# Optimization experiments

Measured on AMD Instinct MI355X. Metric: run time of the kernel, lower is better.

The kernel has to match this reference:

```python
import jax, jax.numpy as jnp
import numpy as np

N = 50000      # nodes
E = 800000     # edges (avg degree 16)
NF = 128       # input feature dim
H = 128        # hidden dim
GAMMA = 1.0    # gm init arg
COS_EPS = 1e-8 # F.cosine_similarity eps
EW_MIN = 1e-4  # edge-weight clamp


def setup_inputs() -> dict:
    key = jax.random.key(0)
    ks = jax.random.split(key, 9)
    x = jax.random.normal(ks[0], (N, NF), dtype=jnp.float32)
    edge_index = jax.random.randint(ks[1], (2, E), 0, N, dtype=jnp.int64)
    sensitive_attr = jax.random.randint(ks[2], (N,), 0, 2, dtype=jnp.int64)
    s1 = 1.0 / np.sqrt(NF)
    s2 = 1.0 / np.sqrt(H)
    W1 = jax.random.normal(ks[3], (NF, H), dtype=jnp.float32) * s1
    b1 = jnp.zeros((H,), dtype=jnp.float32)
    W2 = jax.random.normal(ks[4], (H, H), dtype=jnp.float32) * s2
    b2 = jnp.zeros((H,), dtype=jnp.float32)
    Wc = jax.random.normal(ks[5], (H, 1), dtype=jnp.float32) * s2
    bc = jnp.zeros((1,), dtype=jnp.float32)
    return {"x": x, "edge_index": edge_index, "sensitive_attr": sensitive_attr,
            "W1": W1, "b1": b1, "W2": W2, "b2": b2, "Wc": Wc, "bc": bc}


def gcn_conv(x, W, b, src, dst, ew, n):
    """PyG GCNConv: lin -> symmetric-normalized edge-weighted aggregation (+self loops) -> bias."""
    xt = x @ W                                              # [N,H]
    deg = jax.ops.segment_sum(ew, dst, num_segments=n) + 1.0  # self-loop weight 1
    dinv = jnp.where(deg > 0, deg ** -0.5, 0.0)             # [N]
    norm = dinv[src] * ew * dinv[dst]                       # [E]
    agg = jax.ops.segment_sum(xt[src] * norm[:, None], dst, num_segments=n)
    # self-loop contribution: norm_ii = dinv[i] * 1 * dinv[i]
    return agg + xt * (dinv * dinv)[:, None] + b


def reference(x, edge_index, sensitive_attr, W1, b1, W2, b2, Wc, bc):
    src, dst = edge_index[0], edge_index[1]
    # cosine-similarity edge weights (gather-heavy)
    xs, xd = x[src], x[dst]                                  # [E,F] each
    dot = jnp.sum(xs * xd, axis=1)
    ns = jnp.maximum(jnp.sqrt(jnp.sum(xs * xs, axis=1)), COS_EPS)
    nd = jnp.maximum(jnp.sqrt(jnp.sum(xd * xd, axis=1)), COS_EPS)
    sim = dot / (ns * nd)
    sen_diff = (sensitive_attr[src] != sensitive_attr[dst]).astype(x.dtype)
    ew = jnp.maximum(sim * jnp.exp(-GAMMA * sen_diff), EW_MIN)
    # two GCN layers (dropout is identity in eval mode)
    h = jax.nn.relu(gcn_conv(x, W1, b1, src, dst, ew, N))
    h = jax.nn.relu(gcn_conv(h, W2, b2, src, dst, ew, N))
    y = h @ Wc + bc                                          # [N,1]
    return (y, h)
```

## Files before the change

kernel.cpp:

```cpp
#include <hip/hip_runtime.h>


typedef unsigned short u16;
typedef unsigned int u32;
typedef __attribute__((ext_vector_type(8))) short short8;
typedef __attribute__((ext_vector_type(4))) float floatx4;

__device__ __forceinline__ float bflo(u32 u){ return __uint_as_float(u << 16); }
__device__ __forceinline__ float bfhi(u32 u){ return __uint_as_float(u & 0xFFFF0000u); }
__device__ __forceinline__ float bf1(u16 u){ return __uint_as_float(((u32)u) << 16); }
__device__ __forceinline__ u16 f2bf(float f){
    u32 u = __float_as_uint(f);
    u += 0x7FFFu + ((u >> 16) & 1u);
    return (u16)(u >> 16);
}
__device__ __forceinline__ u32 pack2(float a, float b){
    return (u32)f2bf(a) | ((u32)f2bf(b) << 16);
}
__device__ __forceinline__ float wsum(float v){
#pragma unroll
    for (int o = 32; o > 0; o >>= 1) v += __shfl_xor(v, o, 64);
    return v;
}
__device__ __forceinline__ float ld1(const void* p, size_t idx, int f32){
    return f32 ? ((const float*)p)[idx] : bf1(((const u16*)p)[idx]);
}
__device__ __forceinline__ int ldidx(const int* p, size_t i, int i64){
    return i64 ? p[2 * i] : p[i];
}

__global__ void classify_k(const u32* __restrict__ xw, const int* __restrict__ eiw,
                           int* __restrict__ flags)
{
    __shared__ int c_out, c_nz;
    int t = threadIdx.x;
    if (t == 0) { c_out = 0; c_nz = 0; }
    __syncthreads();
    u32 w = xw[t];
    int e = (w >> 7) & 0xFF;
    int outl = (e < 110 || e > 140) ? 1 : 0;
    int nz = (eiw[2 * t + 1] != 0) ? 1 : 0;
    atomicAdd(&c_out, outl);
    atomicAdd(&c_nz, nz);
    __syncthreads();
    if (t == 0) { flags[0] = (c_out > 256); flags[1] = (c_nz < 256); }
}

__global__ __launch_bounds__(256) void convhist_k(const void* __restrict__ x,
                                                  u32* __restrict__ xb,
                                                  float* __restrict__ rn, int N,
                                                  const int* __restrict__ ei,
                                                  int* __restrict__ cnt, int E,
                                                  const int* __restrict__ flags,
                                                  int nbN)
{
    if ((int)blockIdx.x < nbN) {
        int i = blockIdx.x * 4 + (threadIdx.x >> 6);
        if (i >= N) return;
        int lane = threadIdx.x & 63;
        u32 u;
        if (flags[0]) {
            const float* q = (const float*)x + (size_t)i * 128 + lane * 2;
            u = pack2(q[0], q[1]);
        } else u = ((const u32*)x)[(size_t)i * 64 + lane];
        xb[(size_t)i * 64 + lane] = u;
        float f0 = bflo(u), f1 = bfhi(u);
        float ss = wsum(f0 * f0 + f1 * f1);
        if (lane == 0) rn[i] = 1.0f / fmaxf(sqrtf(ss), 1e-8f);
    } else {
        int e = (blockIdx.x - nbN) * 256 + threadIdx.x;
        if (e >= E) return;
        int d = ldidx(ei, (size_t)E + e, flags[1]);
        if ((u32)d >= (u32)N) d = 0;
        atomicAdd(&cnt[d], 1);
    }
}

__global__ void prep_k(const void* __restrict__ W1, const void* __restrict__ W2,
                       uint4* __restrict__ wf1, uint4* __restrict__ wf2,
                       const int* __restrict__ flags)
{
    int slot = blockIdx.x * 256 + threadIdx.x;
    if (slot >= 4096) return;
    int f32w = flags[0];
    const void* W = (slot < 2048) ? W1 : W2;
    uint4* wf = (slot < 2048) ? wf1 : wf2;
    int s = slot & 2047;
    int lane = s & 63, kk = (s >> 6) & 3, ct = s >> 8;
    int q = lane >> 4, n = lane & 15;
    int col = ct * 16 + n, k0 = kk * 32 + q * 8;
    union { u16 us[8]; uint4 u4; } tmp;
#pragma unroll
    for (int j = 0; j < 8; ++j)
        tmp.us[j] = f2bf(ld1(W, (size_t)(k0 + j) * 128 + col, f32w));
    wf[s] = tmp.u4;
}

__global__ __launch_bounds__(256) void scanA_k(int* __restrict__ cnt,
                                               int* __restrict__ rowp,
                                               int* __restrict__ bsum, int N)
{
    __shared__ int wtot[4];
    int t = threadIdx.x, lane = t & 63, w = t >> 6;
    int i0 = blockIdx.x * 1024 + t * 4;
    int v[4];
#pragma unroll
    for (int k = 0; k < 4; ++k) {
        int i = i0 + k;
        v[k] = (i < N) ? cnt[i] : 0;
        if (i < N) cnt[i] = 0;
    }
    int t4 = v[0] + v[1] + v[2] + v[3];
    int sc = t4;
#pragma unroll
    for (int o = 1; o < 64; o <<= 1) {
        int nv = __shfl_up(sc, o);
        if (lane >= o) sc += nv;
    }
    if (lane == 63) wtot[w] = sc;
    __syncthreads();
    int wo = 0, tot = 0;
#pragma unroll
    for (int k = 0; k < 4; ++k) { int s = wtot[k]; if (k < w) wo += s; tot += s; }
    int pre = wo + sc - t4;
#pragma unroll
    for (int k = 0; k < 4; ++k) {
        int i = i0 + k;
        if (i < N) rowp[i] = pre;
        pre += v[k];
    }
    if (t == 0) bsum[blockIdx.x] = tot;
}

__global__ void scanB_k(int* __restrict__ bsum, int* __restrict__ rowp,
                        int nb, int N)
{
    int lane = threadIdx.x;
    int carry = 0;
    for (int base = 0; base < nb; base += 64) {
        int i = base + lane;
        int v = (i < nb) ? bsum[i] : 0;
        int sc = v;
#pragma unroll
        for (int o = 1; o < 64; o <<= 1) {
            int nv = __shfl_up(sc, o);
            if (lane >= o) sc += nv;
        }
        if (i < nb) bsum[i] = carry + sc - v;
        carry += __shfl(sc, 63);
    }
    if (lane == 0) rowp[N] = carry;
}

__global__ __launch_bounds__(256) void scanC_k(int* __restrict__ rowp,
                                               const int* __restrict__ bsum, int N)
{
    int off = bsum[blockIdx.x];
    int i0 = blockIdx.x * 1024 + threadIdx.x * 4;
#pragma unroll
    for (int k = 0; k < 4; ++k) {
        int i = i0 + k;
        if (i < N) rowp[i] += off;
    }
}

__global__ __launch_bounds__(256) void ewscat_k(const u32* __restrict__ xb,
                                                const float* __restrict__ rn,
                                                const int* __restrict__ ei,
                                                const int* __restrict__ sa,
                                                const int* __restrict__ rowp,
                                                int* __restrict__ cnt,
                                                u32* __restrict__ rec,
                                                float* __restrict__ degacc,
                                                int E, int N,
                                                const int* __restrict__ flags)
{
    int t = threadIdx.x;
    int lane = t & 63;
    int g = lane >> 4, j = lane & 15;
    int wid = (blockIdx.x * 256 + t) >> 6;
    int eb = wid * 16;
    int i64 = flags[1];
    int sArr[4], dArr[4];
    bool ok[4];
#pragma unroll
    for (int k = 0; k < 4; ++k) {
        int e = eb + k * 4 + g;
        ok[k] = e < E;
        int s = 0, d = 0;
        if (ok[k]) {
            s = ldidx(ei, e, i64); d = ldidx(ei, (size_t)E + e, i64);
            if ((u32)s >= (u32)N) s = 0;
            if ((u32)d >= (u32)N) d = 0;
        }
        sArr[k] = s; dArr[k] = d;
    }
    uint4 A[4], B[4];
#pragma unroll
    for (int k = 0; k < 4; ++k) {
        A[k] = ((const uint4*)(xb + (size_t)sArr[k] * 64))[j];
        B[k] = ((const uint4*)(xb + (size_t)dArr[k] * 64))[j];
    }
    float dot[4];
#pragma unroll
    for (int k = 0; k < 4; ++k) {
        dot[k] = bflo(A[k].x) * bflo(B[k].x) + bfhi(A[k].x) * bfhi(B[k].x)
               + bflo(A[k].y) * bflo(B[k].y) + bfhi(A[k].y) * bfhi(B[k].y)
               + bflo(A[k].z) * bflo(B[k].z) + bfhi(A[k].z) * bfhi(B[k].z)
               + bflo(A[k].w) * bflo(B[k].w) + bfhi(A[k].w) * bfhi(B[k].w);
    }
#pragma unroll
    for (int o = 8; o > 0; o >>= 1) {
#pragma unroll
        for (int k = 0; k < 4; ++k) dot[k] += __shfl_xor(dot[k], o);
    }
    if (j == 0) {
#pragma unroll
        for (int k = 0; k < 4; ++k) {
            if (!ok[k]) continue;
            int s = sArr[k], d = dArr[k];
            float sim = dot[k] * rn[s] * rn[d];
            int as_ = i64 ? sa[2 * (size_t)s] : sa[s];
            int ad_ = i64 ? sa[2 * (size_t)d] : sa[d];
            float f = (as_ != ad_) ? 0.36787944117144233f : 1.0f;
            float w = fmaxf(sim * f, 1e-4f);
            int pos = rowp[d] + atomicAdd(&cnt[d], 1);
            if ((u32)pos >= (u32)E) pos = 0;
            rec[pos] = ((u32)s << 16) | f2bf(w);
            atomicAdd(&degacc[d], w);
        }
    }
}

__global__ __launch_bounds__(256) void dinv_k(float* __restrict__ dv, int N)
{
    int i = blockIdx.x * 256 + threadIdx.x;
    if (i < N) dv[i] = 1.0f / sqrtf(1.0f + dv[i]);
}

__global__ __launch_bounds__(256) void agg_k(const u32* __restrict__ feat,
                                             const int* __restrict__ rowp,
                                             const u32* __restrict__ rec,
                                             const float* __restrict__ dinv,
                                             u32* __restrict__ Tb, int N, int E)
{
    int i = blockIdx.x * 4 + (threadIdx.x >> 6);
    if (i >= N) return;
    int lane = threadIdx.x & 63;
    float di = dinv[i], sc = di * di;
    u32 u = feat[(size_t)i * 64 + lane];
    float a0 = bflo(u) * sc, a1 = bfhi(u) * sc;
    int p0 = rowp[i], p1 = rowp[i + 1];
    if (p0 < 0) p0 = 0;
    if (p1 > E) p1 = E;
    int p = p0;
    for (; p + 7 < p1; p += 8) {
        u32 r[8]; int s[8]; u32 v[8];
#pragma unroll
        for (int k = 0; k < 8; ++k) {
            r[k] = rec[p + k];
            s[k] = r[k] >> 16;
            if (s[k] >= N) s[k] = 0;
        }
#pragma unroll
        for (int k = 0; k < 8; ++k) v[k] = feat[(size_t)s[k] * 64 + lane];
#pragma unroll
        for (int k = 0; k < 8; ++k) {
            float w = bf1((u16)r[k]) * di * dinv[s[k]];
            a0 = fmaf(w, bflo(v[k]), a0);
            a1 = fmaf(w, bfhi(v[k]), a1);
        }
    }
    for (; p + 1 < p1; p += 2) {
        u32 r0 = rec[p], r1 = rec[p + 1];
        int s0 = r0 >> 16, s1 = r1 >> 16;
        if (s0 >= N) s0 = 0;
        if (s1 >= N) s1 = 0;
        u32 v0 = feat[(size_t)s0 * 64 + lane];
        u32 v1 = feat[(size_t)s1 * 64 + lane];
        float w0 = bf1((u16)r0) * di * dinv[s0];
        float w1 = bf1((u16)r1) * di * dinv[s1];
        a0 = fmaf(w0, bflo(v0), a0); a1 = fmaf(w0, bfhi(v0), a1);
        a0 = fmaf(w1, bflo(v1), a0); a1 = fmaf(w1, bfhi(v1), a1);
    }
    if (p < p1) {
        u32 r0 = rec[p];
        int s0 = r0 >> 16;
        if (s0 >= N) s0 = 0;
        u32 v0 = feat[(size_t)s0 * 64 + lane];
        float w0 = bf1((u16)r0) * di * dinv[s0];
        a0 = fmaf(w0, bflo(v0), a0); a1 = fmaf(w0, bfhi(v0), a1);
    }
    Tb[(size_t)i * 64 + lane] = pack2(a0, a1);
}

__global__ __launch_bounds__(256) void gemm_m(const u32* __restrict__ Tb,
                                              const uint4* __restrict__ wfrag,
                                              const void* __restrict__ bias,
                                              void* __restrict__ out, int outbf,
                                              int N,
                                              const void* __restrict__ Wc,
                                              const void* __restrict__ bc,
                                              float* __restrict__ yout,
                                              const int* __restrict__ flags)
{
    int t = threadIdx.x, wave = t >> 6, lane = t & 63;
    int q = lane >> 4, n = lane & 15;
    int f32w = flags[0];
    int rowbase = blockIdx.x * 64 + wave * 16;
    int arow = rowbase + n; if (arow > N - 1) arow = N - 1;
    const uint4* ap = (const uint4*)(Tb + (size_t)arow * 64);
    short8 a[4];
#pragma unroll
    for (int kk = 0; kk < 4; ++kk) {
        uint4 av = ap[kk * 4 + q];
        a[kk] = *(short8*)&av;
    }
    floatx4 acc[8];
#pragma unroll
    for (int ct = 0; ct < 8; ++ct) acc[ct] = (floatx4){0.f, 0.f, 0.f, 0.f};
#pragma unroll
    for (int ct = 0; ct < 8; ++ct) {
#pragma unroll
        for (int kk = 0; kk < 4; ++kk) {
            uint4 bv = wfrag[(ct * 4 + kk) * 64 + lane];
            acc[ct] = __builtin_amdgcn_mfma_f32_16x16x32_bf16(
                a[kk], *(short8*)&bv, acc[ct], 0, 0, 0);
        }
    }
    float bcv = 0.0f;
    float part[4] = {0.f, 0.f, 0.f, 0.f};
    if (yout) bcv = ld1(bc, 0, f32w);
#pragma unroll
    for (int ct = 0; ct < 8; ++ct) {
        int col = ct * 16 + n;
        float bia = ld1(bias, col, f32w);
        float wcv = yout ? ld1(Wc, col, f32w) : 0.0f;
#pragma unroll
        for (int r = 0; r < 4; ++r) {
            int row = rowbase + q * 4 + r;
            float h = fmaxf(acc[ct][r] + bia, 0.0f);
            if (row < N) {
                if (outbf) ((u16*)out)[(size_t)row * 128 + col] = f2bf(h);
                else       ((float*)out)[(size_t)row * 128 + col] = h;
            }
            part[r] = fmaf(h, wcv, part[r]);
        }
    }
    if (yout) {
#pragma unroll
        for (int r = 0; r < 4; ++r) {
            float pr = part[r];
#pragma unroll
            for (int o = 8; o > 0; o >>= 1) pr += __shfl_xor(pr, o);
            int row = rowbase + q * 4 + r;
            if (n == 0 && row < N) yout[row] = pr + bcv;
        }
    }
}

extern "C" void kernel_launch(void* const* d_in, const int* in_sizes, int n_in,
                              void* d_out, int out_size, void* d_ws, size_t ws_size,
                              hipStream_t stream)
{
    const void* x  = d_in[0];
    const int* ei  = (const int*)d_in[1];
    const int* sa  = (const int*)d_in[2];
    const void* W1 = d_in[3];
    const void* b1 = d_in[4];
    const void* W2 = d_in[5];
    const void* b2 = d_in[6];
    const void* Wc = d_in[7];
    const void* bc = d_in[8];
    const int N = in_sizes[2];
    const int E = in_sizes[1] / 2;

    float* y_out = (float*)d_out;
    float* h_out = y_out + N;
    u32*   Tbuf  = (u32*)d_in[0];

    const int nbN = (N + 3) / 4, nbE = (E + 255) / 256;
    const int nbS = (N + 1023) / 1024;

    char* p = (char*)d_ws;
    auto carve = [&](size_t bytes) { char* r = p; p += (bytes + 255) & ~(size_t)255; return r; };
    int*   flags = (int*)carve(256);
    float* rn    = (float*)carve((size_t)N * 4);
    float* dinv  = (float*)carve((size_t)N * 4);
    int*   cnt   = (int*)carve((size_t)N * 4);
    int*   rowp  = (int*)carve((size_t)(N + 1) * 4);
    int*   bsum  = (int*)carve((size_t)nbS * 4);
    uint4* wf1   = (uint4*)carve(2048 * 16);
    uint4* wf2   = (uint4*)carve(2048 * 16);
    u32*   rec   = (u32*)carve((size_t)E * 4);
    u32*   xb    = (u32*)carve((size_t)N * 64 * 4);

    classify_k<<<1, 1024, 0, stream>>>((const u32*)x, ei, flags);
    hipMemsetAsync(dinv, 0, (size_t)N * 4, stream);
    hipMemsetAsync(cnt, 0, (size_t)N * 4, stream);
    convhist_k<<<nbN + nbE, 256, 0, stream>>>(x, xb, rn, N, ei, cnt, E, flags, nbN);
    prep_k<<<16, 256, 0, stream>>>(W1, W2, wf1, wf2, flags);
    scanA_k<<<nbS, 256, 0, stream>>>(cnt, rowp, bsum, N);
    scanB_k<<<1, 64, 0, stream>>>(bsum, rowp, nbS, N);
    scanC_k<<<nbS, 256, 0, stream>>>(rowp, bsum, N);
    ewscat_k<<<(E + 63) / 64, 256, 0, stream>>>(xb, rn, ei, sa, rowp, cnt,
                                                rec, dinv, E, N, flags);
    dinv_k<<<(N + 255) / 256, 256, 0, stream>>>(dinv, N);

    agg_k<<<(N + 3) / 4, 256, 0, stream>>>(xb, rowp, rec, dinv, Tbuf, N, E);
    gemm_m<<<(N + 63) / 64, 256, 0, stream>>>(Tbuf, wf1, b1, xb, 1, N,
                                              nullptr, nullptr, nullptr, flags);
    agg_k<<<(N + 3) / 4, 256, 0, stream>>>(xb, rowp, rec, dinv, Tbuf, N, E);
    gemm_m<<<(N + 63) / 64, 256, 0, stream>>>(Tbuf, wf2, b2, h_out, 0, N,
                                              Wc, bc, y_out, flags);
}
```

Measured before the change: 336.1 us.

## Fold sensitive attr into norm sign, compute degree from CSR, fuse weight prep

Encodes each node's sensitive attribute in the sign of its reciprocal norm, so the edge-weight kernel no longer gathers the attribute array. The per-edge float atomicAdd into the degree accumulator is removed; dinv_k now sums the bf16 edge weights per row from the CSR records. That also drops a memset, and it changes rounding because the degree is now summed from bf16-rounded weights. Weight prep is merged into the convert/histogram launch, and the edge kernel handles 2 edges per 16-lane group instead of 4, which halves per-thread work and doubles the grid.

```diff
diff --git a/kernel.cpp b/kernel.cpp
--- a/kernel.cpp
+++ b/kernel.cpp
@@ -50,12 +50,18 @@
                                                   u32* __restrict__ xb,
                                                   float* __restrict__ rn, int N,
                                                   const int* __restrict__ ei,
+                                                  const int* __restrict__ sa,
                                                   int* __restrict__ cnt, int E,
+                                                  const void* __restrict__ W1,
+                                                  const void* __restrict__ W2,
+                                                  uint4* __restrict__ wf1,
+                                                  uint4* __restrict__ wf2,
                                                   const int* __restrict__ flags,
-                                                  int nbN)
-{
-    if ((int)blockIdx.x < nbN) {
-        int i = blockIdx.x * 4 + (threadIdx.x >> 6);
+                                                  int nbN, int nbE)
+{
+    int b = blockIdx.x;
+    if (b < nbN) {
+        int i = b * 4 + (threadIdx.x >> 6);
         if (i >= N) return;
         int lane = threadIdx.x & 63;
         u32 u;
@@ -66,34 +72,33 @@
         xb[(size_t)i * 64 + lane] = u;
         float f0 = bflo(u), f1 = bfhi(u);
         float ss = wsum(f0 * f0 + f1 * f1);
-        if (lane == 0) rn[i] = 1.0f / fmaxf(sqrtf(ss), 1e-8f);
-    } else {
-        int e = (blockIdx.x - nbN) * 256 + threadIdx.x;
+        if (lane == 0) {
+            float r = 1.0f / fmaxf(sqrtf(ss), 1e-8f);
+            int a = flags[1] ? sa[2 * (size_t)i] : sa[i];
+            rn[i] = a ? -r : r;
+        }
+    } else if (b < nbN + nbE) {
+        int e = (b - nbN) * 256 + threadIdx.x;
         if (e >= E) return;
         int d = ldidx(ei, (size_t)E + e, flags[1]);
         if ((u32)d >= (u32)N) d = 0;
         atomicAdd(&cnt[d], 1);
-    }
-}
-
-__global__ void prep_k(const void* __restrict__ W1, const void* __restrict__ W2,
-                       uint4* __restrict__ wf1, uint4* __restrict__ wf2,
-                       const int* __restrict__ flags)
-{
-    int slot = blockIdx.x * 256 + threadIdx.x;
-    if (slot >= 4096) return;
-    int f32w = flags[0];
-    const void* W = (slot < 2048) ? W1 : W2;
-    uint4* wf = (slot < 2048) ? wf1 : wf2;
-    int s = slot & 2047;
-    int lane = s & 63, kk = (s >> 6) & 3, ct = s >> 8;
-    int q = lane >> 4, n = lane & 15;
-    int col = ct * 16 + n, k0 = kk * 32 + q * 8;
-    union { u16 us[8]; uint4 u4; } tmp;
-#pragma unroll
-    for (int j = 0; j < 8; ++j)
-        tmp.us[j] = f2bf(ld1(W, (size_t)(k0 + j) * 128 + col, f32w));
-    wf[s] = tmp.u4;
+    } else {
+        int slot = (b - nbN - nbE) * 256 + threadIdx.x;
+        if (slot >= 4096) return;
+        int f32w = flags[0];
+        const void* W = (slot < 2048) ? W1 : W2;
+        uint4* wf = (slot < 2048) ? wf1 : wf2;
+        int s = slot & 2047;
+        int lane = s & 63, kk = (s >> 6) & 3, ct = s >> 8;
+        int q = lane >> 4, n = lane & 15;
+        int col = ct * 16 + n, k0 = kk * 32 + q * 8;
+        union { u16 us[8]; uint4 u4; } tmp;
+#pragma unroll
+        for (int j = 0; j < 8; ++j)
+            tmp.us[j] = f2bf(ld1(W, (size_t)(k0 + j) * 128 + col, f32w));
+        wf[s] = tmp.u4;
+    }
 }
 
 __global__ __launch_bounds__(256) void scanA_k(int* __restrict__ cnt,
@@ -167,75 +172,81 @@
 __global__ __launch_bounds__(256) void ewscat_k(const u32* __restrict__ xb,
                                                 const float* __restrict__ rn,
                                                 const int* __restrict__ ei,
-                                                const int* __restrict__ sa,
                                                 const int* __restrict__ rowp,
                                                 int* __restrict__ cnt,
                                                 u32* __restrict__ rec,
-                                                float* __restrict__ degacc,
                                                 int E, int N,
                                                 const int* __restrict__ flags)
 {
     int t = threadIdx.x;
-    int lane = t & 63;
+    int lane = t & 63, wave = t >> 6;
     int g = lane >> 4, j = lane & 15;
-    int wid = (blockIdx.x * 256 + t) >> 6;
-    int eb = wid * 16;
+    int wid = blockIdx.x * 4 + wave;
+    int e0 = wid * 8 + g, e1 = e0 + 4;
     int i64 = flags[1];
-    int sArr[4], dArr[4];
-    bool ok[4];
-#pragma unroll
-    for (int k = 0; k < 4; ++k) {
-        int e = eb + k * 4 + g;
-        ok[k] = e < E;
-        int s = 0, d = 0;
-        if (ok[k]) {
-            s = ldidx(ei, e, i64); d = ldidx(ei, (size_t)E + e, i64);
-            if ((u32)s >= (u32)N) s = 0;
-            if ((u32)d >= (u32)N) d = 0;
-        }
-        sArr[k] = s; dArr[k] = d;
-    }
-    uint4 A[4], B[4];
-#pragma unroll
-    for (int k = 0; k < 4; ++k) {
-        A[k] = ((const uint4*)(xb + (size_t)sArr[k] * 64))[j];
-        B[k] = ((const uint4*)(xb + (size_t)dArr[k] * 64))[j];
-    }
-    float dot[4];
-#pragma unroll
-    for (int k = 0; k < 4; ++k) {
-        dot[k] = bflo(A[k].x) * bflo(B[k].x) + bfhi(A[k].x) * bfhi(B[k].x)
-               + bflo(A[k].y) * bflo(B[k].y) + bfhi(A[k].y) * bfhi(B[k].y)
-               + bflo(A[k].z) * bflo(B[k].z) + bfhi(A[k].z) * bfhi(B[k].z)
-               + bflo(A[k].w) * bflo(B[k].w) + bfhi(A[k].w) * bfhi(B[k].w);
-    }
+    int s0 = 0, d0 = 0, s1 = 0, d1 = 0;
+    bool ok0 = e0 < E, ok1 = e1 < E;
+    if (ok0) {
+        s0 = ldidx(ei, e0, i64); d0 = ldidx(ei, (size_t)E + e0, i64);
+        if ((u32)s0 >= (u32)N) s0 = 0;
+        if ((u32)d0 >= (u32)N) d0 = 0;
+    }
+    if (ok1) {
+        s1 = ldidx(ei, e1, i64); d1 = ldidx(ei, (size_t)E + e1, i64);
+        if ((u32)s1 >= (u32)N) s1 = 0;
+        if ((u32)d1 >= (u32)N) d1 = 0;
+    }
+    uint4 A0 = ((const uint4*)(xb + (size_t)s0 * 64))[j];
+    uint4 B0 = ((const uint4*)(xb + (size_t)d0 * 64))[j];
+    uint4 A1 = ((const uint4*)(xb + (size_t)s1 * 64))[j];
+    uint4 B1 = ((const uint4*)(xb + (size_t)d1 * 64))[j];
+    float dot0 = bflo(A0.x) * bflo(B0.x) + bfhi(A0.x) * bfhi(B0.x)
+               + bflo(A0.y) * bflo(B0.y) + bfhi(A0.y) * bfhi(B0.y)
+               + bflo(A0.z) * bflo(B0.z) + bfhi(A0.z) * bfhi(B0.z)
+               + bflo(A0.w) * bflo(B0.w) + bfhi(A0.w) * bfhi(B0.w);
+    float dot1 = bflo(A1.x) * bflo(B1.x) + bfhi(A1.x) * bfhi(B1.x)
+               + bflo(A1.y) * bflo(B1.y) + bfhi(A1.y) * bfhi(B1.y)
+               + bflo(A1.z) * bflo(B1.z) + bfhi(A1.z) * bfhi(B1.z)
+               + bflo(A1.w) * bflo(B1.w) + bfhi(A1.w) * bfhi(B1.w);
 #pragma unroll
     for (int o = 8; o > 0; o >>= 1) {
-#pragma unroll
-        for (int k = 0; k < 4; ++k) dot[k] += __shfl_xor(dot[k], o);
+        dot0 += __shfl_xor(dot0, o);
+        dot1 += __shfl_xor(dot1, o);
     }
     if (j == 0) {
-#pragma unroll
-        for (int k = 0; k < 4; ++k) {
-            if (!ok[k]) continue;
-            int s = sArr[k], d = dArr[k];
-            float sim = dot[k] * rn[s] * rn[d];
-            int as_ = i64 ? sa[2 * (size_t)s] : sa[s];
-            int ad_ = i64 ? sa[2 * (size_t)d] : sa[d];
-            float f = (as_ != ad_) ? 0.36787944117144233f : 1.0f;
+        if (ok0) {
+            float prod = rn[s0] * rn[d0];
+            float sim = dot0 * fabsf(prod);
+            float f = (prod < 0.0f) ? 0.36787944117144233f : 1.0f;
             float w = fmaxf(sim * f, 1e-4f);
-            int pos = rowp[d] + atomicAdd(&cnt[d], 1);
+            int pos = rowp[d0] + atomicAdd(&cnt[d0], 1);
             if ((u32)pos >= (u32)E) pos = 0;
-            rec[pos] = ((u32)s << 16) | f2bf(w);
-            atomicAdd(&degacc[d], w);
-        }
-    }
-}
-
-__global__ __launch_bounds__(256) void dinv_k(float* __restrict__ dv, int N)
+            rec[pos] = ((u32)s0 << 16) | f2bf(w);
+        }
+        if (ok1) {
+            float prod = rn[s1] * rn[d1];
+            float sim = dot1 * fabsf(prod);
+            float f = (prod < 0.0f) ? 0.36787944117144233f : 1.0f;
+            float w = fmaxf(sim * f, 1e-4f);
+            int pos = rowp[d1] + atomicAdd(&cnt[d1], 1);
+            if ((u32)pos >= (u32)E) pos = 0;
+            rec[pos] = ((u32)s1 << 16) | f2bf(w);
+        }
+    }
+}
+
+__global__ __launch_bounds__(256) void dinv_k(const int* __restrict__ rowp,
+                                              const u32* __restrict__ rec,
+                                              float* __restrict__ dv, int N, int E)
 {
     int i = blockIdx.x * 256 + threadIdx.x;
-    if (i < N) dv[i] = 1.0f / sqrtf(1.0f + dv[i]);
+    if (i >= N) return;
+    int p0 = rowp[i], p1 = rowp[i + 1];
+    if (p0 < 0) p0 = 0;
+    if (p1 > E) p1 = E;
+    float s = 1.0f;
+    for (int p = p0; p < p1; ++p) s += bf1((u16)rec[p]);
+    dv[i] = 1.0f / sqrtf(s);
 }
 
 __global__ __launch_bounds__(256) void agg_k(const u32* __restrict__ feat,
@@ -396,16 +407,16 @@
     u32*   xb    = (u32*)carve((size_t)N * 64 * 4);
 
     classify_k<<<1, 1024, 0, stream>>>((const u32*)x, ei, flags);
-    hipMemsetAsync(dinv, 0, (size_t)N * 4, stream);
     hipMemsetAsync(cnt, 0, (size_t)N * 4, stream);
-    convhist_k<<<nbN + nbE, 256, 0, stream>>>(x, xb, rn, N, ei, cnt, E, flags, nbN);
-    prep_k<<<16, 256, 0, stream>>>(W1, W2, wf1, wf2, flags);
+    convhist_k<<<nbN + nbE + 16, 256, 0, stream>>>(x, xb, rn, N, ei, sa, cnt, E,
+                                                   W1, W2, wf1, wf2, flags,
+                                                   nbN, nbE);
     scanA_k<<<nbS, 256, 0, stream>>>(cnt, rowp, bsum, N);
     scanB_k<<<1, 64, 0, stream>>>(bsum, rowp, nbS, N);
     scanC_k<<<nbS, 256, 0, stream>>>(rowp, bsum, N);
-    ewscat_k<<<(E + 63) / 64, 256, 0, stream>>>(xb, rn, ei, sa, rowp, cnt,
-                                                rec, dinv, E, N, flags);
-    dinv_k<<<(N + 255) / 256, 256, 0, stream>>>(dinv, N);
+    ewscat_k<<<(E + 31) / 32, 256, 0, stream>>>(xb, rn, ei, rowp, cnt,
+                                                rec, E, N, flags);
+    dinv_k<<<(N + 255) / 256, 256, 0, stream>>>(rowp, rec, dinv, N, E);
 
     agg_k<<<(N + 3) / 4, 256, 0, stream>>>(xb, rowp, rec, dinv, Tbuf, N, E);
     gemm_m<<<(N + 63) / 64, 256, 0, stream>>>(Tbuf, wf1, b1, xb, 1, N,
```

Result: faster. 310.5 us (-7.6%).
